# Kernel optimization log

Measured on AMD Instinct MI355X. Metric: run time of the kernel, lower is better.

The kernel has to match this reference:

```python
import jax, jax.numpy as jnp
import numpy as np

NC, NQ, BOX = 20, 27, 6  # classes, queries-per-class, 3D box dim (cx,cy,cz,w,h,d)
COST_CLASS, COST_BBOX, COST_GIOU = 2.0, 5.0, 2.0


def box_cxcyczwhd_to_xyzxyz(b):
    c, s = b[..., :3], b[..., 3:]
    return jnp.concatenate([c - 0.5 * s, c + 0.5 * s], axis=-1)


def giou3d_vs_single(pred, tgt):
    # pred: [B,NC,NQ,6] xyzxyz, tgt: [B,NC,6] xyzxyz -> giou [B,NC,NQ]
    vol_p = jnp.prod(pred[..., 3:] - pred[..., :3], -1)            # [B,NC,NQ]
    vol_t = jnp.prod(tgt[..., 3:] - tgt[..., :3], -1)[..., None]   # [B,NC,1]
    t = tgt[..., None, :]                                          # [B,NC,1,6]
    lt = jnp.maximum(pred[..., :3], t[..., :3])
    rb = jnp.minimum(pred[..., 3:], t[..., 3:])
    inter = jnp.prod(jnp.clip(rb - lt, 0.0), -1)                   # [B,NC,NQ]
    union = vol_p + vol_t - inter
    iou = inter / union
    lt2 = jnp.minimum(pred[..., :3], t[..., :3])
    rb2 = jnp.maximum(pred[..., 3:], t[..., 3:])
    hull = jnp.prod(jnp.clip(rb2 - lt2, 0.0), -1)
    return iou - (hull - union) / hull


def setup_inputs() -> dict:
    key = jax.random.key(0)
    k1, k2, k3, k4 = jax.random.split(key, 4)
    bs = 8192
    return {
        "pred_logits": jax.random.normal(k1, (bs, NC * NQ, 1), dtype=jnp.float32),
        "pred_boxes": jax.random.uniform(k2, (bs, NC * NQ, BOX), dtype=jnp.float32),
        "tgt_boxes": jax.random.uniform(k3, (bs, NC, BOX), dtype=jnp.float32),
        "tgt_present": jax.random.randint(k4, (bs, NC), 0, 2, dtype=jnp.int32),
        "num_top_queries": 1,
    }


def reference(pred_logits, pred_boxes, tgt_boxes, tgt_present, num_top_queries):
    bs = pred_logits.shape[0]
    boxes = pred_boxes.reshape(bs, NC, NQ, BOX).astype(jnp.float32)
    logits = pred_logits.reshape(bs, NC, NQ).astype(jnp.float32)

    cost_class = -jax.nn.sigmoid(logits)                                   # [B,NC,NQ]
    cost_bbox = jnp.sum(jnp.abs(boxes - tgt_boxes[:, :, None, :]), -1)      # L1 cdist, [B,NC,NQ]
    giou = giou3d_vs_single(box_cxcyczwhd_to_xyzxyz(jnp.clip(boxes, 0.0)),
                            box_cxcyczwhd_to_xyzxyz(tgt_boxes))
    cost_giou = -giou                                                       # [B,NC,NQ]

    C = COST_BBOX * cost_bbox + COST_CLASS * cost_class + COST_GIOU * cost_giou

    _, idx = jax.lax.top_k(-C, num_top_queries)                             # smallest-k, [B,NC,k]
    onehot = jax.nn.one_hot(idx, NQ, dtype=jnp.int32).sum(-2)               # [B,NC,NQ]
    present = tgt_present.astype(bool)[..., None]                           # [B,NC,1]
    matches = jnp.where(present, (onehot > 0).astype(jnp.int32), 0)

    gmax = cost_giou.max(-1, keepdims=True)
    gmin = cost_giou.min(-1, keepdims=True)
    soft = jnp.clip((cost_giou - gmax) / (gmin - gmax), 0.0)
    soft_labels = jnp.where(present, soft, -1.0)
    return matches, soft_labels
```

## Files before the change

kernel.cpp:

```cpp
#include <hip/hip_runtime.h>
#include <hip/hip_bf16.h>
#include <math.h>

#define NCC 20
#define NQQ 27
#define BSZ 8192
#define NPAIR (BSZ * NCC)
#define PPB 32

__device__ __forceinline__ float frcp(float x) { return __builtin_amdgcn_rcpf(x); }

struct Tgt {
    float tc0, tc1, tc2, tw, th, td;
    float tl0, tl1, tl2, th0, th1, th2, vol;
};

__device__ __forceinline__ Tgt make_tgt(float2 t01, float2 t23, float2 t45) {
    Tgt T;
    T.tc0 = t01.x; T.tc1 = t01.y; T.tc2 = t23.x;
    T.tw  = t23.y; T.th  = t45.x; T.td  = t45.y;
    T.tl0 = T.tc0 - 0.5f * T.tw; T.tl1 = T.tc1 - 0.5f * T.th; T.tl2 = T.tc2 - 0.5f * T.td;
    T.th0 = T.tc0 + 0.5f * T.tw; T.th1 = T.tc1 + 0.5f * T.th; T.th2 = T.tc2 + 0.5f * T.td;
    T.vol = (T.th0 - T.tl0) * (T.th1 - T.tl1) * (T.th2 - T.tl2);
    return T;
}

__device__ __forceinline__ float pair_cost(float2 b01, float2 b23, float2 b45,
                                           float lg, const Tgt& T, float* cg) {
    const float bc0 = b01.x, bc1 = b01.y, bc2 = b23.x;
    const float bw  = b23.y, bh  = b45.x, bd  = b45.y;

    const float cost_class = -frcp(1.0f + __expf(-lg));

    const float cost_bbox =
        fabsf(bc0 - T.tc0) + fabsf(bc1 - T.tc1) + fabsf(bc2 - T.tc2) +
        fabsf(bw  - T.tw ) + fabsf(bh  - T.th ) + fabsf(bd  - T.td );

    const float cc0 = fmaxf(bc0, 0.0f), cc1 = fmaxf(bc1, 0.0f), cc2 = fmaxf(bc2, 0.0f);
    const float cw  = fmaxf(bw , 0.0f), ch  = fmaxf(bh , 0.0f), cd  = fmaxf(bd , 0.0f);
    const float pl0 = cc0 - 0.5f * cw, pl1 = cc1 - 0.5f * ch, pl2 = cc2 - 0.5f * cd;
    const float ph0 = cc0 + 0.5f * cw, ph1 = cc1 + 0.5f * ch, ph2 = cc2 + 0.5f * cd;
    const float vol_p = (ph0 - pl0) * (ph1 - pl1) * (ph2 - pl2);

    const float i0 = fmaxf(fminf(ph0, T.th0) - fmaxf(pl0, T.tl0), 0.0f);
    const float i1 = fmaxf(fminf(ph1, T.th1) - fmaxf(pl1, T.tl1), 0.0f);
    const float i2 = fmaxf(fminf(ph2, T.th2) - fmaxf(pl2, T.tl2), 0.0f);
    const float inter = i0 * i1 * i2;
    const float uni   = vol_p + T.vol - inter;
    const float iou   = inter * frcp(uni);

    const float h0 = fmaxf(fmaxf(ph0, T.th0) - fminf(pl0, T.tl0), 0.0f);
    const float h1 = fmaxf(fmaxf(ph1, T.th1) - fminf(pl1, T.tl1), 0.0f);
    const float h2 = fmaxf(fmaxf(ph2, T.th2) - fminf(pl2, T.tl2), 0.0f);
    const float hull = h0 * h1 * h2;

    const float giou = iou - (hull - uni) * frcp(hull);
    *cg = -giou;
    return 5.0f * cost_bbox + 2.0f * cost_class + 2.0f * (-giou);
}

__global__ __launch_bounds__(256, 6) void matcher_kernel(
    const float* __restrict__ logits,
    const float* __restrict__ boxes,
    const float* __restrict__ tboxes,
    const int*   __restrict__ present,
    float* __restrict__ out_matches,
    float* __restrict__ out_soft)
{
    __shared__ float sBox[PPB * 162];
    __shared__ float sLog[PPB * NQQ];
    __shared__ float sTgt[PPB * 6];
    __shared__ int   sPres[PPB];

    const int tid = threadIdx.x;
    const size_t pairBase = (size_t)blockIdx.x * PPB;

    {
        const float4* srcB = reinterpret_cast<const float4*>(boxes + pairBase * 162);
        float4* dstB = reinterpret_cast<float4*>(sBox);
#pragma unroll
        for (int i = 0; i < 5; ++i) dstB[i * 256 + tid] = srcB[i * 256 + tid];
        if (tid < 16) dstB[1280 + tid] = srcB[1280 + tid];

        if (tid < 216) reinterpret_cast<float4*>(sLog)[tid] =
            reinterpret_cast<const float4*>(logits + pairBase * NQQ)[tid];
        if (tid < 48)  reinterpret_cast<float4*>(sTgt)[tid] =
            reinterpret_cast<const float4*>(tboxes + pairBase * 6)[tid];
        if (tid < PPB) sPres[tid] = present[pairBase + tid];
    }
    __syncthreads();

    const int lp = tid >> 3;
    const int l  = tid & 7;
    const int q0 = l * 4;

    const int qa = (q0 + 0 < NQQ) ? q0 + 0 : NQQ - 1;
    const int qb = (q0 + 1 < NQQ) ? q0 + 1 : NQQ - 1;
    const int qc = (q0 + 2 < NQQ) ? q0 + 2 : NQQ - 1;
    const int qd = (q0 + 3 < NQQ) ? q0 + 3 : NQQ - 1;

    const float* bp = sBox + lp * 162;
    float2 a01 = *reinterpret_cast<const float2*>(bp + qa * 6 + 0);
    float2 a23 = *reinterpret_cast<const float2*>(bp + qa * 6 + 2);
    float2 a45 = *reinterpret_cast<const float2*>(bp + qa * 6 + 4);
    float2 b01 = *reinterpret_cast<const float2*>(bp + qb * 6 + 0);
    float2 b23 = *reinterpret_cast<const float2*>(bp + qb * 6 + 2);
    float2 b45 = *reinterpret_cast<const float2*>(bp + qb * 6 + 4);
    float2 c01 = *reinterpret_cast<const float2*>(bp + qc * 6 + 0);
    float2 c23 = *reinterpret_cast<const float2*>(bp + qc * 6 + 2);
    float2 c45 = *reinterpret_cast<const float2*>(bp + qc * 6 + 4);
    float2 d01 = *reinterpret_cast<const float2*>(bp + qd * 6 + 0);
    float2 d23 = *reinterpret_cast<const float2*>(bp + qd * 6 + 2);
    float2 d45 = *reinterpret_cast<const float2*>(bp + qd * 6 + 4);
    const float* lpg = sLog + lp * NQQ;
    const float lga = lpg[qa], lgb = lpg[qb], lgc = lpg[qc], lgd = lpg[qd];
    const float* tp = sTgt + lp * 6;
    float2 t01 = *reinterpret_cast<const float2*>(tp + 0);
    float2 t23 = *reinterpret_cast<const float2*>(tp + 2);
    float2 t45 = *reinterpret_cast<const float2*>(tp + 4);
    const int pres = sPres[lp];

    const Tgt T = make_tgt(t01, t23, t45);

    const bool va = (q0 + 0 < NQQ), vb = (q0 + 1 < NQQ),
               vc = (q0 + 2 < NQQ), vd = (q0 + 3 < NQQ);

    float cg0, cg1, cg2, cg3;
    float C0 = pair_cost(a01, a23, a45, lga, T, &cg0);
    float C1 = pair_cost(b01, b23, b45, lgb, T, &cg1);
    float C2 = pair_cost(c01, c23, c45, lgc, T, &cg2);
    float C3 = pair_cost(d01, d23, d45, lgd, T, &cg3);
    if (!va) C0 = INFINITY;
    if (!vb) C1 = INFINITY;
    if (!vc) C2 = INFINITY;
    if (!vd) C3 = INFINITY;

    float bestC = C0; int bestj = 0;
    if (C1 < bestC) { bestC = C1; bestj = 1; }
    if (C2 < bestC) { bestC = C2; bestj = 2; }
    if (C3 < bestC) { bestC = C3; bestj = 3; }
    float gx = va ? cg0 : -INFINITY;
    float gn = va ? cg0 :  INFINITY;
    if (vb) { gx = fmaxf(gx, cg1); gn = fminf(gn, cg1); }
    if (vc) { gx = fmaxf(gx, cg2); gn = fminf(gn, cg2); }
    if (vd) { gx = fmaxf(gx, cg3); gn = fminf(gn, cg3); }

    float m = bestC;
#pragma unroll
    for (int s = 4; s >= 1; s >>= 1) {
        m  = fminf(m,  __shfl_xor(m,  s, 8));
        gx = fmaxf(gx, __shfl_xor(gx, s, 8));
        gn = fminf(gn, __shfl_xor(gn, s, 8));
    }

    const unsigned long long bal = __ballot(bestC == m);
    const int gbase  = (tid & 63) & ~7;
    const unsigned int gbits = (unsigned int)(bal >> gbase) & 0xFFu;
    const int winner = __ffs(gbits) - 1;
    const bool mine  = (winner == l);

    __syncthreads();
    float* sOutM = sBox;
    float* sOutS = sBox + PPB * NQQ;

    const float inv = frcp(gn - gx);
    float* smM = sOutM + lp * NQQ + q0;
    float* smS = sOutS + lp * NQQ + q0;
    if (va) { smM[0] = (pres && mine && bestj == 0) ? 1.0f : 0.0f;
              smS[0] = pres ? fmaxf((cg0 - gx) * inv, 0.0f) : -1.0f; }
    if (vb) { smM[1] = (pres && mine && bestj == 1) ? 1.0f : 0.0f;
              smS[1] = pres ? fmaxf((cg1 - gx) * inv, 0.0f) : -1.0f; }
    if (vc) { smM[2] = (pres && mine && bestj == 2) ? 1.0f : 0.0f;
              smS[2] = pres ? fmaxf((cg2 - gx) * inv, 0.0f) : -1.0f; }
    if (vd) { smM[3] = (pres && mine && bestj == 3) ? 1.0f : 0.0f;
              smS[3] = pres ? fmaxf((cg3 - gx) * inv, 0.0f) : -1.0f; }
    __syncthreads();

    if (tid < 216) {
        const float4 vM = reinterpret_cast<const float4*>(sOutM)[tid];
        const float4 vS = reinterpret_cast<const float4*>(sOutS)[tid];
        reinterpret_cast<float4*>(out_matches + pairBase * NQQ)[tid] = vM;
        reinterpret_cast<float4*>(out_soft    + pairBase * NQQ)[tid] = vS;
    }
}

extern "C" void kernel_launch(void* const* d_in, const int* in_sizes, int n_in,
                              void* d_out, int out_size, void* d_ws, size_t ws_size,
                              hipStream_t stream) {
    const float* logits  = (const float*)d_in[0];
    const float* boxes   = (const float*)d_in[1];
    const float* tboxes  = (const float*)d_in[2];
    const int*   presnt  = (const int*)d_in[3];

    float* out = (float*)d_out;
    float* out_matches = out;
    float* out_soft    = out + (size_t)NPAIR * NQQ;

    dim3 block(256);
    dim3 grid(NPAIR / PPB);
    matcher_kernel<<<grid, block, 0, stream>>>(logits, boxes, tboxes, presnt,
                                               out_matches, out_soft);
}
```

Before: 32.66 us.

## Load boxes via global_load_lds and read logits/targets directly from global

Box data now moves from global memory straight into LDS using the global_load_lds builtin (16-byte per lane), skipping the round trip through registers. Logits, target boxes and presence flags are read per thread directly from global memory instead of being staged in shared memory, which shrinks the LDS footprint. The launch-bounds occupancy hint rises from 6 to 7 blocks. The risks are uncoalesced, redundant per-lane global reads for logits and targets, and reliance on 16-byte direct-to-LDS support; a plain __syncthreads may also not reliably wait for the asynchronous LDS loads to finish.

```diff
diff --git a/kernel.cpp b/kernel.cpp
--- a/kernel.cpp
+++ b/kernel.cpp
@@ -7,6 +7,9 @@
 #define BSZ 8192
 #define NPAIR (BSZ * NCC)
 #define PPB 32
+
+typedef __attribute__((address_space(1))) const float gfloat;
+typedef __attribute__((address_space(3))) float lfloat;
 
 __device__ __forceinline__ float frcp(float x) { return __builtin_amdgcn_rcpf(x); }
 
@@ -59,7 +62,7 @@
     return 5.0f * cost_bbox + 2.0f * cost_class + 2.0f * (-giou);
 }
 
-__global__ __launch_bounds__(256, 6) void matcher_kernel(
+__global__ __launch_bounds__(256, 7) void matcher_kernel(
     const float* __restrict__ logits,
     const float* __restrict__ boxes,
     const float* __restrict__ tboxes,
@@ -68,36 +71,42 @@
     float* __restrict__ out_soft)
 {
     __shared__ float sBox[PPB * 162];
-    __shared__ float sLog[PPB * NQQ];
-    __shared__ float sTgt[PPB * 6];
-    __shared__ int   sPres[PPB];
 
     const int tid = threadIdx.x;
     const size_t pairBase = (size_t)blockIdx.x * PPB;
-
-    {
-        const float4* srcB = reinterpret_cast<const float4*>(boxes + pairBase * 162);
-        float4* dstB = reinterpret_cast<float4*>(sBox);
+    const float* gB = boxes + pairBase * 162;
+
 #pragma unroll
-        for (int i = 0; i < 5; ++i) dstB[i * 256 + tid] = srcB[i * 256 + tid];
-        if (tid < 16) dstB[1280 + tid] = srcB[1280 + tid];
-
-        if (tid < 216) reinterpret_cast<float4*>(sLog)[tid] =
-            reinterpret_cast<const float4*>(logits + pairBase * NQQ)[tid];
-        if (tid < 48)  reinterpret_cast<float4*>(sTgt)[tid] =
-            reinterpret_cast<const float4*>(tboxes + pairBase * 6)[tid];
-        if (tid < PPB) sPres[tid] = present[pairBase + tid];
-    }
-    __syncthreads();
+    for (int i = 0; i < 5; ++i) {
+        __builtin_amdgcn_global_load_lds(
+            (gfloat*)(gB   + (size_t)(i * 256 + tid) * 4),
+            (lfloat*)(sBox + (size_t)(i * 256 + tid) * 4),
+            16, 0, 0);
+    }
+    if (tid < 16) {
+        reinterpret_cast<float4*>(sBox)[1280 + tid] =
+            reinterpret_cast<const float4*>(gB)[1280 + tid];
+    }
 
     const int lp = tid >> 3;
     const int l  = tid & 7;
     const int q0 = l * 4;
+    const size_t p = pairBase + lp;
 
     const int qa = (q0 + 0 < NQQ) ? q0 + 0 : NQQ - 1;
     const int qb = (q0 + 1 < NQQ) ? q0 + 1 : NQQ - 1;
     const int qc = (q0 + 2 < NQQ) ? q0 + 2 : NQQ - 1;
     const int qd = (q0 + 3 < NQQ) ? q0 + 3 : NQQ - 1;
+
+    const float* lpg = logits + p * NQQ;
+    const float lga = lpg[qa], lgb = lpg[qb], lgc = lpg[qc], lgd = lpg[qd];
+    const float* tp_ = tboxes + p * 6;
+    float2 t01 = *reinterpret_cast<const float2*>(tp_ + 0);
+    float2 t23 = *reinterpret_cast<const float2*>(tp_ + 2);
+    float2 t45 = *reinterpret_cast<const float2*>(tp_ + 4);
+    const int pres = present[p];
+
+    __syncthreads();
 
     const float* bp = sBox + lp * 162;
     float2 a01 = *reinterpret_cast<const float2*>(bp + qa * 6 + 0);
@@ -112,13 +121,6 @@
     float2 d01 = *reinterpret_cast<const float2*>(bp + qd * 6 + 0);
     float2 d23 = *reinterpret_cast<const float2*>(bp + qd * 6 + 2);
     float2 d45 = *reinterpret_cast<const float2*>(bp + qd * 6 + 4);
-    const float* lpg = sLog + lp * NQQ;
-    const float lga = lpg[qa], lgb = lpg[qb], lgc = lpg[qc], lgd = lpg[qd];
-    const float* tp = sTgt + lp * 6;
-    float2 t01 = *reinterpret_cast<const float2*>(tp + 0);
-    float2 t23 = *reinterpret_cast<const float2*>(tp + 2);
-    float2 t45 = *reinterpret_cast<const float2*>(tp + 4);
-    const int pres = sPres[lp];
 
     const Tgt T = make_tgt(t01, t23, t45);
 
```

Measured after the change: 30.81 us. -5.7%, faster.
